# Performance work log

Measured on AMD Instinct MI355X. Metric: run time of the kernel, lower is better.

Reference implementation:

```python
import jax, jax.numpy as jnp
import numpy as np

# Mamba2 defaults (mamba_ssm): d_state=64, d_conv=4, expand=2, headdim=64, ngroups=1
D_MODEL = 512
D_STATE = 64
D_CONV = 4
EXPAND = 2
HEADDIM = 64
D_INNER = EXPAND * D_MODEL            # 1024
NHEADS = D_INNER // HEADDIM           # 16
CONV_DIM = D_INNER + 2 * D_STATE      # 1152
D_IN_PROJ = 2 * D_INNER + 2 * D_STATE + NHEADS  # 2192
BATCH, SEQLEN, CHUNK = 4, 4096, 64


def setup_inputs() -> dict:
    key = jax.random.key(0)
    ks = jax.random.split(key, 8)
    return {
        "x": jax.random.normal(ks[0], (BATCH, SEQLEN, D_MODEL), jnp.float32),
        "ln_w": jnp.ones((D_MODEL,), jnp.float32),
        "ln_b": jnp.zeros((D_MODEL,), jnp.float32),
        "in_w": jax.random.normal(ks[1], (D_MODEL, D_IN_PROJ), jnp.float32) * (D_MODEL ** -0.5),
        "conv_w": jax.random.normal(ks[2], (CONV_DIM, D_CONV), jnp.float32) * (D_CONV ** -0.5),
        "conv_b": jnp.zeros((CONV_DIM,), jnp.float32),
        "dt_bias": jnp.log(jnp.expm1(jax.random.uniform(ks[3], (NHEADS,), jnp.float32, 0.001, 0.1))),
        "A_log": jnp.log(jax.random.uniform(ks[4], (NHEADS,), jnp.float32, 1.0, 16.0)),
        "D": jnp.ones((NHEADS,), jnp.float32),
        "rms_w": jnp.ones((D_INNER,), jnp.float32),
        "out_w": jax.random.normal(ks[5], (D_INNER, D_MODEL), jnp.float32) * (D_INNER ** -0.5),
    }


def _layernorm(x, w, b, eps=1e-5):
    mu = jnp.mean(x, axis=-1, keepdims=True)
    var = jnp.mean((x - mu) ** 2, axis=-1, keepdims=True)
    return (x - mu) * jax.lax.rsqrt(var + eps) * w + b


def _causal_dwconv(x, w, b):  # x [B,L,C], w [C,K], b [C]
    K = w.shape[1]
    xp = jnp.pad(x, ((0, 0), (K - 1, 0), (0, 0)))
    L = x.shape[1]
    out = sum(xp[:, k:k + L, :] * w[None, None, :, k] for k in range(K))
    return out + b


def _ssd(xh, dt, Bm, Cm, A):
    # Chunked SSD (Mamba2 algorithm). xh [B,L,H,P], dt [B,L,H], Bm/Cm [B,L,N], A [H] (negative)
    b, l, h, p = xh.shape
    nc, cs = l // CHUNK, CHUNK
    Xd = (xh * dt[..., None]).reshape(b, nc, cs, h, p)
    Bc = Bm.reshape(b, nc, cs, -1)
    Cc = Cm.reshape(b, nc, cs, -1)
    Ac = (dt * A).reshape(b, nc, cs, h).transpose(0, 3, 1, 2)  # [B,H,nC,cs]
    Acum = jnp.cumsum(Ac, axis=-1)                              # [B,H,nC,cs]
    # intra-chunk (diagonal blocks)
    mask = jnp.tril(jnp.ones((cs, cs), bool))
    seg = Acum[..., :, None] - Acum[..., None, :]               # [B,H,nC,cs,cs]
    Lmat = jnp.where(mask, jnp.exp(jnp.where(mask, seg, 0.0)), 0.0)
    Y_diag = jnp.einsum('bcln,bcsn,bhcls,bcshp->bclhp', Cc, Bc, Lmat, Xd)
    # per-chunk end states
    decay = jnp.exp(Acum[..., -1:] - Acum)                      # [B,H,nC,cs]
    states = jnp.einsum('bcln,bhcl,bclhp->bchpn', Bc, decay, Xd)  # [B,nC,H,P,N]
    chunk_decay = jnp.exp(Acum[..., -1])                        # [B,H,nC]
    def step(s, inp):
        st_c, dec_c = inp
        prev = s
        s = s * dec_c[..., None, None] + st_c
        return s, prev
    _, prev = jax.lax.scan(
        step,
        jnp.zeros((b, h, p, Bc.shape[-1]), xh.dtype),
        (states.transpose(1, 0, 2, 3, 4), chunk_decay.transpose(2, 0, 1)),
    )
    prev = prev.transpose(1, 0, 2, 3, 4)                        # [B,nC,H,P,N]
    Y_off = jnp.einsum('bcln,bchpn,bhcl->bclhp', Cc, prev, jnp.exp(Acum))
    return (Y_diag + Y_off).reshape(b, l, h, p)


def reference(x, ln_w, ln_b, in_w, conv_w, conv_b, dt_bias, A_log, D, rms_w, out_w):
    b, l, _ = x.shape
    h = _layernorm(x, ln_w, ln_b)
    zxbcdt = h @ in_w                                           # [B,L,D_IN_PROJ]
    z = zxbcdt[..., :D_INNER]
    xBC = zxbcdt[..., D_INNER:D_INNER + CONV_DIM]
    dt = jax.nn.softplus(zxbcdt[..., -NHEADS:] + dt_bias)       # [B,L,H]
    xBC = jax.nn.silu(_causal_dwconv(xBC, conv_w, conv_b))
    xs = xBC[..., :D_INNER]
    Bm = xBC[..., D_INNER:D_INNER + D_STATE]
    Cm = xBC[..., D_INNER + D_STATE:]
    xh = xs.reshape(b, l, NHEADS, HEADDIM)
    A = -jnp.exp(A_log)                                         # [H]
    y = _ssd(xh, dt, Bm, Cm, A) + xh * D[None, None, :, None]
    y = y.reshape(b, l, D_INNER)
    # gated RMSNorm: rmsnorm(y * silu(z)) * rms_w
    g = y * jax.nn.silu(z)
    g = g * jax.lax.rsqrt(jnp.mean(g * g, axis=-1, keepdims=True) + 1e-5) * rms_w
    out = g @ out_w
    # dropout in eval mode = identity, drop_path=0 = identity
    return x + out
```

## Files before the change

### kernel.cpp

```cpp
#include <hip/hip_runtime.h>
#include <hip/hip_bf16.h>
#include <cstddef>

#define BATCH  4
#define SEQL   4096
#define DM     512
#define DIP    2192
#define DIPP   2304
#define DI     1024
#define DST    64
#define NH     16
#define HD     64
#define CONVD  1152
#define NROWS  (BATCH*SEQL)

typedef __attribute__((ext_vector_type(8))) short short8;
typedef __attribute__((ext_vector_type(4))) float f32x4;

__device__ __forceinline__ float silu_f(float v){ return v/(1.f+__expf(-v)); }

__device__ __forceinline__ unsigned short bf16_rne(float x){
  unsigned u = __float_as_uint(x);
  unsigned r = u + 0x7FFFu + ((u>>16)&1u);
  return (unsigned short)(r>>16);
}
__device__ __forceinline__ float bf16_to_f(unsigned short h){
  return __uint_as_float(((unsigned)h)<<16);
}

__global__ __launch_bounds__(256)
void k_stats(const float* __restrict__ x, float* __restrict__ stats){
  __shared__ float sm[8];
  int row = blockIdx.x, t = threadIdx.x;
  const float* xr = x + (size_t)row*DM;
  float v0 = xr[t], v1 = xr[t+256];
  float s = v0+v1, s2 = v0*v0+v1*v1;
  for(int o=32;o;o>>=1){ s += __shfl_down(s,o); s2 += __shfl_down(s2,o); }
  if((t&63)==0){ sm[t>>6]=s; sm[4+(t>>6)]=s2; }
  __syncthreads();
  if(t==0){
    float su = sm[0]+sm[1]+sm[2]+sm[3];
    float sq = sm[4]+sm[5]+sm[6]+sm[7];
    float mu = su*(1.f/DM);
    float rs = rsqrtf(sq*(1.f/DM) - mu*mu + 1e-5f);
    stats[row*2] = mu; stats[row*2+1] = rs;
  }
}

__global__ void k_wsplit(const float* __restrict__ src, unsigned short* __restrict__ dh,
                         unsigned short* __restrict__ dl, int K, int N){
  __shared__ float sm[32][33];
  int tx = threadIdx.x, ty = threadIdx.y;
  int n0 = blockIdx.x*32, k0 = blockIdx.y*32;
  #pragma unroll
  for(int j=0;j<4;j++){
    int k = k0+ty+j*8, n = n0+tx;
    sm[ty+j*8][tx] = (k<K && n<N) ? src[(size_t)k*N+n] : 0.f;
  }
  __syncthreads();
  #pragma unroll
  for(int j=0;j<4;j++){
    int n = n0+ty+j*8, k = k0+tx;
    float v = sm[tx][ty+j*8];
    unsigned short hh = bf16_rne(v);
    dh[(size_t)n*K+k] = hh;
    dl[(size_t)n*K+k] = bf16_rne(v - bf16_to_f(hh));
  }
}

__global__ __launch_bounds__(256)
void k_gemm_in(const float* __restrict__ x, const float* __restrict__ stats,
               const float* __restrict__ lnw, const float* __restrict__ lnb,
               const unsigned short* __restrict__ Bhg, const unsigned short* __restrict__ Blg,
               float* __restrict__ z, float* __restrict__ xbc){
  __shared__ unsigned short Ah[128][72], Al[128][72], Bh[128][72], Bl[128][72];
  const int ntn = DIPP/128;
  int bid = blockIdx.x;
  int tm = bid / ntn, tn = bid % ntn;
  int t = threadIdx.x, lane = t&63, wave = t>>6;
  int wr = (wave>>1)*64, wc = (wave&1)*64, fr = lane&15;
  f32x4 zero = {0.f,0.f,0.f,0.f};
  f32x4 acc[4][4];
  #pragma unroll
  for(int m=0;m<4;m++)
    #pragma unroll
    for(int n=0;n<4;n++) acc[m][n]=zero;
  const int arow = tm*128, bcol = tn*128;
  for(int k0=0; k0<DM; k0+=64){
    __syncthreads();
    #pragma unroll
    for(int i=0;i<8;i++){
      int idx = t + i*256;
      int r = idx>>4, cq = (idx&15)*4;
      int grow = arow + r;
      f32x4 xv = *(const f32x4*)(x + (size_t)grow*DM + k0 + cq);
      float mu = stats[grow*2], rsd = stats[grow*2+1];
      f32x4 wv = *(const f32x4*)(lnw + k0 + cq);
      f32x4 bv = *(const f32x4*)(lnb + k0 + cq);
      #pragma unroll
      for(int j=0;j<4;j++){
        float v = (xv[j]-mu)*rsd*wv[j] + bv[j];
        unsigned short hh = bf16_rne(v);
        Ah[r][cq+j] = hh;
        Al[r][cq+j] = bf16_rne(v - bf16_to_f(hh));
      }
    }
    #pragma unroll
    for(int i=0;i<4;i++){
      int idx = t + i*256;
      int r = idx>>3, c8 = (idx&7)*8;
      *(short8*)(&Bh[r][c8]) = *(const short8*)(Bhg + (size_t)(bcol+r)*DM + k0 + c8);
      *(short8*)(&Bl[r][c8]) = *(const short8*)(Blg + (size_t)(bcol+r)*DM + k0 + c8);
    }
    __syncthreads();
    #pragma unroll
    for(int kk=0;kk<2;kk++){
      int fk = kk*32 + ((lane>>4)<<3);
      short8 afh[4], afl[4], bfh[4], bfl[4];
      #pragma unroll
      for(int m=0;m<4;m++){
        afh[m] = *(const short8*)(&Ah[wr+m*16+fr][fk]);
        afl[m] = *(const short8*)(&Al[wr+m*16+fr][fk]);
      }
      #pragma unroll
      for(int n=0;n<4;n++){
        bfh[n] = *(const short8*)(&Bh[wc+n*16+fr][fk]);
        bfl[n] = *(const short8*)(&Bl[wc+n*16+fr][fk]);
      }
      #pragma unroll
      for(int m=0;m<4;m++)
        #pragma unroll
        for(int n=0;n<4;n++){
          acc[m][n] = __builtin_amdgcn_mfma_f32_16x16x32_bf16(afh[m], bfh[n], acc[m][n], 0,0,0);
          acc[m][n] = __builtin_amdgcn_mfma_f32_16x16x32_bf16(afh[m], bfl[n], acc[m][n], 0,0,0);
          acc[m][n] = __builtin_amdgcn_mfma_f32_16x16x32_bf16(afl[m], bfh[n], acc[m][n], 0,0,0);
        }
    }
  }
  int fq = (lane>>4)*4;
  #pragma unroll
  for(int m=0;m<4;m++)
    #pragma unroll
    for(int n=0;n<4;n++)
      #pragma unroll
      for(int j=0;j<4;j++){
        int row = arow + wr + m*16 + fq + j;
        int col = bcol + wc + n*16 + fr;
        float v = acc[m][n][j];
        if(col < DI) z[(size_t)row*DI + col] = v;
        else if(col < DI+CONVD) xbc[(size_t)row*CONVD + (col-DI)] = v;
      }
}

__global__ __launch_bounds__(256)
void k_gemm_out(const float* __restrict__ G, const unsigned short* __restrict__ Bhg,
                const unsigned short* __restrict__ Blg, const float* __restrict__ resid,
                float* __restrict__ outp){
  __shared__ unsigned short Ah[128][72], Al[128][72], Bh[128][72], Bl[128][72];
  const int ntn = DM/128;
  int bid = blockIdx.x;
  int tm = bid / ntn, tn = bid % ntn;
  int t = threadIdx.x, lane = t&63, wave = t>>6;
  int wr = (wave>>1)*64, wc = (wave&1)*64, fr = lane&15;
  f32x4 zero = {0.f,0.f,0.f,0.f};
  f32x4 acc[4][4];
  #pragma unroll
  for(int m=0;m<4;m++)
    #pragma unroll
    for(int n=0;n<4;n++) acc[m][n]=zero;
  const int arow = tm*128, bcol = tn*128;
  for(int k0=0; k0<DI; k0+=64){
    __syncthreads();
    int h = k0>>6;
    #pragma unroll
    for(int i=0;i<8;i++){
      int idx = t + i*256;
      int r = idx>>4, cq = (idx&15)*4;
      int grow = arow + r;
      int bb = grow>>12, cc = (grow>>6)&63, lin = grow&63;
      size_t base = ((size_t)((bb*64+cc)*NH + h))*4096 + (size_t)lin*64;
      f32x4 gv = *(const f32x4*)(G + base + cq);
      #pragma unroll
      for(int j=0;j<4;j++){
        unsigned short hh = bf16_rne(gv[j]);
        Ah[r][cq+j] = hh;
        Al[r][cq+j] = bf16_rne(gv[j] - bf16_to_f(hh));
      }
    }
    #pragma unroll
    for(int i=0;i<4;i++){
      int idx = t + i*256;
      int r = idx>>3, c8 = (idx&7)*8;
      *(short8*)(&Bh[r][c8]) = *(const short8*)(Bhg + (size_t)(bcol+r)*DI + k0 + c8);
      *(short8*)(&Bl[r][c8]) = *(const short8*)(Blg + (size_t)(bcol+r)*DI + k0 + c8);
    }
    __syncthreads();
    #pragma unroll
    for(int kk=0;kk<2;kk++){
      int fk = kk*32 + ((lane>>4)<<3);
      short8 afh[4], afl[4], bfh[4], bfl[4];
      #pragma unroll
      for(int m=0;m<4;m++){
        afh[m] = *(const short8*)(&Ah[wr+m*16+fr][fk]);
        afl[m] = *(const short8*)(&Al[wr+m*16+fr][fk]);
      }
      #pragma unroll
      for(int n=0;n<4;n++){
        bfh[n] = *(const short8*)(&Bh[wc+n*16+fr][fk]);
        bfl[n] = *(const short8*)(&Bl[wc+n*16+fr][fk]);
      }
      #pragma unroll
      for(int m=0;m<4;m++)
        #pragma unroll
        for(int n=0;n<4;n++){
          acc[m][n] = __builtin_amdgcn_mfma_f32_16x16x32_bf16(afh[m], bfh[n], acc[m][n], 0,0,0);
          acc[m][n] = __builtin_amdgcn_mfma_f32_16x16x32_bf16(afh[m], bfl[n], acc[m][n], 0,0,0);
          acc[m][n] = __builtin_amdgcn_mfma_f32_16x16x32_bf16(afl[m], bfh[n], acc[m][n], 0,0,0);
        }
    }
  }
  int fq = (lane>>4)*4;
  #pragma unroll
  for(int m=0;m<4;m++)
    #pragma unroll
    for(int n=0;n<4;n++)
      #pragma unroll
      for(int j=0;j<4;j++){
        int row = arow + wr + m*16 + fq + j;
        int col = bcol + wc + n*16 + fr;
        outp[(size_t)row*DM + col] = acc[m][n][j] + resid[(size_t)row*DM + col];
      }
}

__global__ __launch_bounds__(256)
void k_dt(const float* __restrict__ x, const float* __restrict__ stats,
          const float* __restrict__ lnw, const float* __restrict__ lnb,
          const float* __restrict__ in_w, const float* __restrict__ dt_bias,
          float* __restrict__ dtp){
  __shared__ float red[64];
  int row = blockIdx.x, t = threadIdx.x;
  float mu = stats[row*2], rs = stats[row*2+1];
  float a[16];
  #pragma unroll
  for(int j=0;j<16;j++) a[j]=0.f;
  #pragma unroll
  for(int i=0;i<2;i++){
    int k = t + i*256;
    float hv = (x[(size_t)row*DM + k]-mu)*rs*lnw[k] + lnb[k];
    const float* wr2 = in_w + (size_t)k*DIP + (DIP-NH);
    #pragma unroll
    for(int j=0;j<16;j++) a[j] += hv * wr2[j];
  }
  for(int o=32;o;o>>=1){
    #pragma unroll
    for(int j=0;j<16;j++) a[j] += __shfl_down(a[j],o);
  }
  if((t&63)==0){
    #pragma unroll
    for(int j=0;j<16;j++) red[(t>>6)*16+j] = a[j];
  }
  __syncthreads();
  if(t<16){
    float v = red[t] + red[16+t] + red[32+t] + red[48+t] + dt_bias[t];
    dtp[(size_t)row*NH + t] = (v > 20.f) ? v : log1pf(__expf(v));
  }
}

__global__ __launch_bounds__(256)
void k_convBC(const float* __restrict__ xbc, const float* __restrict__ cw,
              const float* __restrict__ cb, float* __restrict__ bcc){
  int gid = blockIdx.x*256 + threadIdx.x;
  int c4 = gid & 31, row = gid >> 5;
  int c = c4*4;
  int lb = row & (SEQL-1);
  const float* base = xbc + (size_t)row*CONVD + DI + c;
  f32x4 w0 = *(const f32x4*)(cw + (size_t)(DI+c+0)*4);
  f32x4 w1 = *(const f32x4*)(cw + (size_t)(DI+c+1)*4);
  f32x4 w2 = *(const f32x4*)(cw + (size_t)(DI+c+2)*4);
  f32x4 w3 = *(const f32x4*)(cw + (size_t)(DI+c+3)*4);
  f32x4 r = { cb[DI+c], cb[DI+c+1], cb[DI+c+2], cb[DI+c+3] };
  #pragma unroll
  for(int k=0;k<4;k++){
    if(lb-3+k >= 0){
      f32x4 xv = *(const f32x4*)(base + (long)(k-3)*CONVD);
      r.x += xv.x*w0[k]; r.y += xv.y*w1[k]; r.z += xv.z*w2[k]; r.w += xv.w*w3[k];
    }
  }
  r.x = silu_f(r.x); r.y = silu_f(r.y); r.z = silu_f(r.z); r.w = silu_f(r.w);
  *(f32x4*)(bcc + (size_t)row*128 + c) = r;
}

__global__ void k_acum(const float* __restrict__ dtp, const float* __restrict__ A_log,
                       float* __restrict__ acum, float* __restrict__ cdec){
  int bh = blockIdx.x;
  int h = bh & 15;
  int c = blockIdx.y, l = threadIdx.x;
  int row = (bh>>4)*SEQL + c*64 + l;
  float a = -__expf(A_log[h]);
  float v = dtp[(size_t)row*NH + h] * a;
  for(int o=1;o<64;o<<=1){ float u = __shfl_up(v,o); if(l>=o) v += u; }
  acum[(size_t)bh*SEQL + c*64 + l] = v;
  if(l==63) cdec[bh*64 + c] = __expf(v);
}

__global__ __launch_bounds__(256)
void k_states(const float* __restrict__ xbc, const float* __restrict__ bcc,
              const float* __restrict__ dtp, const float* __restrict__ acum,
              const float* __restrict__ cw, const float* __restrict__ cb,
              float* __restrict__ S){
  int h = blockIdx.x, bc = blockIdx.y;
  int b = bc >> 6, c = bc & 63;
  __shared__ float Bd[64][68];
  __shared__ float Xs[64][68];
  __shared__ float raw[67*64];
  __shared__ f32x4 wc4[64];
  __shared__ float cbv[64], acs[64], dts[64];
  int t = threadIdx.x;
  if(t < 64){
    acs[t] = acum[((size_t)(b*NH+h))*SEQL + c*64 + t];
    dts[t] = dtp[(size_t)(b*SEQL + c*64 + t)*NH + h];
    wc4[t] = *(const f32x4*)(cw + (size_t)(h*HD + t)*4);
    cbv[t] = cb[h*HD + t];
  }
  __syncthreads();
  #pragma unroll
  for(int i=0;i<4;i++){
    int idx = t + i*256;
    int l = idx>>4, n4 = (idx&15)*4;
    f32x4 bv = *(const f32x4*)(bcc + (size_t)(b*SEQL + c*64 + l)*128 + n4);
    float dec = __expf(acs[63] - acs[l]);
    *(f32x4*)&Bd[l][n4] = bv * dec;
  }
  #pragma unroll
  for(int i=0;i<5;i++){
    int idx = t + i*256;
    if(idx < 67*16){
      int rr = idx>>4, p4 = (idx&15)*4;
      int wb = c*64 - 3 + rr;
      f32x4 xv = {0.f,0.f,0.f,0.f};
      if(wb >= 0) xv = *(const f32x4*)(xbc + (size_t)(b*SEQL + wb)*CONVD + h*HD + p4);
      *(f32x4*)&raw[rr*64 + p4] = xv;
    }
  }
  __syncthreads();
  {
    int l = t>>2, q = t&3;
    float dtv = dts[l];
    #pragma unroll
    for(int jj=0;jj<16;jj++){
      int p = q*16 + jj;
      f32x4 w = wc4[p];
      float a = cbv[p] + raw[(l+0)*64+p]*w.x + raw[(l+1)*64+p]*w.y
              + raw[(l+2)*64+p]*w.z + raw[(l+3)*64+p]*w.w;
      Xs[l][p] = silu_f(a) * dtv;
    }
  }
  __syncthreads();
  int n = t>>2, p0 = (t&3)*16;
  f32x4 a0={0.f,0.f,0.f,0.f}, a1=a0, a2=a0, a3=a0;
  #pragma unroll 2
  for(int ll=0; ll<64; ll++){
    float bnd = Bd[ll][n];
    const float* xp = &Xs[ll][p0];
    a0 += bnd * *(const f32x4*)(xp);
    a1 += bnd * *(const f32x4*)(xp+4);
    a2 += bnd * *(const f32x4*)(xp+8);
    a3 += bnd * *(const f32x4*)(xp+12);
  }
  float* op = S + ((size_t)(bc*NH + h))*4096 + n*64 + p0;
  *(f32x4*)(op)    = a0;
  *(f32x4*)(op+4)  = a1;
  *(f32x4*)(op+8)  = a2;
  *(f32x4*)(op+12) = a3;
}

__global__ void k_scan(float* __restrict__ S, const float* __restrict__ cdec){
  int g = blockIdx.x*256 + threadIdx.x;
  int bh = g >> 12;
  int pn = g & 4095;
  int b = bh >> 4, h = bh & 15;
  const float* cd = cdec + bh*64;
  float s = 0.f;
  for(int c=0;c<64;c++){
    size_t idx = ((size_t)((b*64 + c)*NH + h))*4096 + pn;
    float v = S[idx];
    float d = cd[c];
    S[idx] = s;
    s = s*d + v;
  }
}

__global__ __launch_bounds__(256)
void k_y(const float* __restrict__ xbc, const float* __restrict__ bcc,
         const float* __restrict__ dtp, const float* __restrict__ acum,
         const float* __restrict__ cw, const float* __restrict__ cb,
         const float* __restrict__ Dp, float* __restrict__ Sreg){
  int h = blockIdx.x, bc = blockIdx.y;
  int b = bc >> 6, c = bc & 63;
  __shared__ float Cs[64][68];
  __shared__ float BM[64][68];
  __shared__ float Xr[64][68];
  __shared__ float PsRaw[64*68];
  __shared__ f32x4 wc4[64];
  __shared__ float cbv[64], acs[64], dts[64];
  int t = threadIdx.x;
  float* Sslot = Sreg + ((size_t)(bc*NH + h))*4096;
  if(t < 64){
    acs[t] = acum[((size_t)(b*NH+h))*SEQL + c*64 + t];
    dts[t] = dtp[(size_t)(b*SEQL + c*64 + t)*NH + h];
    wc4[t] = *(const f32x4*)(cw + (size_t)(h*HD + t)*4);
    cbv[t] = cb[h*HD + t];
  }
  #pragma unroll
  for(int i=0;i<4;i++){
    int idx = t + i*256;
    int l = idx>>4, n4 = (idx&15)*4;
    const float* bp = bcc + (size_t)(b*SEQL + c*64 + l)*128;
    *(f32x4*)&BM[l][n4] = *(const f32x4*)(bp + n4);
    *(f32x4*)&Cs[l][n4] = *(const f32x4*)(bp + 64 + n4);
  }
  #pragma unroll
  for(int i=0;i<5;i++){
    int idx = t + i*256;
    if(idx < 67*16){
      int rr = idx>>4, p4 = (idx&15)*4;
      int wb = c*64 - 3 + rr;
      f32x4 xv = {0.f,0.f,0.f,0.f};
      if(wb >= 0) xv = *(const f32x4*)(xbc + (size_t)(b*SEQL + wb)*CONVD + h*HD + p4);
      *(f32x4*)&PsRaw[rr*64 + p4] = xv;
    }
  }
  __syncthreads();
  {
    int l = t>>2, q = t&3;
    #pragma unroll
    for(int jj=0;jj<16;jj++){
      int p = q*16 + jj;
      f32x4 w = wc4[p];
      float a = cbv[p] + PsRaw[(l+0)*64+p]*w.x + PsRaw[(l+1)*64+p]*w.y
              + PsRaw[(l+2)*64+p]*w.z + PsRaw[(l+3)*64+p]*w.w;
      Xr[l][p] = silu_f(a);
    }
  }
  __syncthreads();
  int gl = t & 63, s0 = (t>>6)*16;
  float g[16];
  #pragma unroll
  for(int j=0;j<16;j++) g[j]=0.f;
  #pragma unroll 1
  for(int n4=0;n4<64;n4+=4){
    f32x4 cv = *(const f32x4*)&Cs[gl][n4];
    #pragma unroll
    for(int j=0;j<16;j++){
      f32x4 bv = *(const f32x4*)&BM[s0+j][n4];
      g[j] += cv.x*bv.x + cv.y*bv.y + cv.z*bv.z + cv.w*bv.w;
    }
  }
  __syncthreads();
  {
    float aclg = acs[gl];
    #pragma unroll
    for(int j=0;j<16;j++){
      int s = s0 + j;
      BM[gl][s] = (s <= gl) ? g[j]*__expf(aclg - acs[s])*dts[s] : 0.f;
    }
  }
  #pragma unroll
  for(int i=0;i<4;i++){
    int idx = t + i*256;
    int s = idx>>4, p4 = (idx&15)*4;
    f32x4 pv = *(const f32x4*)(Sslot + s*64 + p4);
    *(f32x4*)&PsRaw[s*68 + p4] = pv;
  }
  __syncthreads();
  {
    int l = t>>2, p0 = (t&3)*16;
    float eal = __expf(acs[l]);
    float Dh = Dp[h];
    const float* xl = &Xr[l][p0];
    f32x4 a0 = Dh * *(const f32x4*)(xl);
    f32x4 a1 = Dh * *(const f32x4*)(xl+4);
    f32x4 a2 = Dh * *(const f32x4*)(xl+8);
    f32x4 a3 = Dh * *(const f32x4*)(xl+12);
    #pragma unroll 2
    for(int s=0;s<64;s++){
      float m = BM[l][s];
      const float* xp = &Xr[s][p0];
      a0 += m * *(const f32x4*)(xp);
      a1 += m * *(const f32x4*)(xp+4);
      a2 += m * *(const f32x4*)(xp+8);
      a3 += m * *(const f32x4*)(xp+12);
    }
    #pragma unroll 2
    for(int s=0;s<64;s++){
      float cv = eal * Cs[l][s];
      const float* pp = &PsRaw[s*68 + p0];
      a0 += cv * *(const f32x4*)(pp);
      a1 += cv * *(const f32x4*)(pp+4);
      a2 += cv * *(const f32x4*)(pp+8);
      a3 += cv * *(const f32x4*)(pp+12);
    }
    float* yp = Sslot + l*64 + p0;
    *(f32x4*)(yp)    = a0;
    *(f32x4*)(yp+4)  = a1;
    *(f32x4*)(yp+8)  = a2;
    *(f32x4*)(yp+12) = a3;
  }
}

__global__ __launch_bounds__(256)
void k_gate(float* __restrict__ Sreg, const float* __restrict__ z,
            const float* __restrict__ rms_w){
  __shared__ float sm[4];
  int row = blockIdx.x, t = threadIdx.x;
  int b = row>>12, cc = (row>>6)&63, lin = row&63;
  int h = t>>4, p = (t&15)*4;
  float* gp = Sreg + ((size_t)((b*64+cc)*NH + h))*4096 + (size_t)lin*64 + p;
  f32x4 yv = *(const f32x4*)gp;
  f32x4 zv = *(const f32x4*)(z + (size_t)row*DI + t*4);
  f32x4 gv;
  gv.x = yv.x * silu_f(zv.x);
  gv.y = yv.y * silu_f(zv.y);
  gv.z = yv.z * silu_f(zv.z);
  gv.w = yv.w * silu_f(zv.w);
  float ss = gv.x*gv.x + gv.y*gv.y + gv.z*gv.z + gv.w*gv.w;
  for(int o=32;o;o>>=1) ss += __shfl_down(ss,o);
  if((t&63)==0) sm[t>>6] = ss;
  __syncthreads();
  float tot = sm[0]+sm[1]+sm[2]+sm[3];
  float scale = rsqrtf(tot*(1.f/DI) + 1e-5f);
  f32x4 wv = *(const f32x4*)(rms_w + t*4);
  gv.x *= scale*wv.x; gv.y *= scale*wv.y; gv.z *= scale*wv.z; gv.w *= scale*wv.w;
  *(f32x4*)gp = gv;
}

extern "C" void kernel_launch(void* const* d_in, const int* in_sizes, int n_in,
                              void* d_out, int out_size, void* d_ws, size_t ws_size,
                              hipStream_t stream) {
  const float* x      = (const float*)d_in[0];
  const float* ln_w   = (const float*)d_in[1];
  const float* ln_b   = (const float*)d_in[2];
  const float* in_w   = (const float*)d_in[3];
  const float* conv_w = (const float*)d_in[4];
  const float* conv_b = (const float*)d_in[5];
  const float* dt_b   = (const float*)d_in[6];
  const float* A_log  = (const float*)d_in[7];
  const float* Dp     = (const float*)d_in[8];
  const float* rms_w  = (const float*)d_in[9];
  const float* out_w  = (const float*)d_in[10];
  float* out = (float*)d_out;
  char* ws = (char*)d_ws;

  size_t o = 0;
  float* stats = (float*)(ws+o);           o += (size_t)NROWS*2*4;
  unsigned short* w1h = (unsigned short*)(ws+o); o += (size_t)DIPP*DM*2;
  unsigned short* w1l = (unsigned short*)(ws+o); o += (size_t)DIPP*DM*2;
  unsigned short* w2h = (unsigned short*)(ws+o); o += (size_t)DM*DI*2;
  unsigned short* w2l = (unsigned short*)(ws+o); o += (size_t)DM*DI*2;
  float* z    = (float*)(ws+o);            o += (size_t)NROWS*DI*4;
  float* xbc  = (float*)(ws+o);            o += (size_t)NROWS*CONVD*4;
  float* dtp  = (float*)(ws+o);            o += (size_t)NROWS*NH*4;
  float* acum = (float*)(ws+o);            o += (size_t)BATCH*NH*SEQL*4;
  float* cdec = (float*)(ws+o);            o += (size_t)BATCH*NH*64*4;
  float* bcc  = (float*)(ws+o);            o += (size_t)NROWS*128*4;
  float* Sreg = (float*)(ws+o);            o += (size_t)BATCH*64*NH*4096*4;
  if(o > ws_size) return;

  k_stats<<<NROWS, 256, 0, stream>>>(x, stats);
  k_wsplit<<<dim3(DIPP/32, DM/32), dim3(32,8), 0, stream>>>(in_w,  w1h, w1l, DM, DIP);
  k_wsplit<<<dim3(DM/32,  DI/32), dim3(32,8), 0, stream>>>(out_w, w2h, w2l, DI, DM);
  k_gemm_in<<<(NROWS/128)*(DIPP/128), 256, 0, stream>>>(x, stats, ln_w, ln_b, w1h, w1l, z, xbc);
  k_dt<<<NROWS, 256, 0, stream>>>(x, stats, ln_w, ln_b, in_w, dt_b, dtp);
  k_convBC<<<(NROWS*32)/256, 256, 0, stream>>>(xbc, conv_w, conv_b, bcc);
  k_acum<<<dim3(BATCH*NH, 64), 64, 0, stream>>>(dtp, A_log, acum, cdec);
  k_states<<<dim3(NH, BATCH*64), 256, 0, stream>>>(xbc, bcc, dtp, acum, conv_w, conv_b, Sreg);
  k_scan<<<(BATCH*NH*4096)/256, 256, 0, stream>>>(Sreg, cdec);
  k_y<<<dim3(NH, BATCH*64), 256, 0, stream>>>(xbc, bcc, dtp, acum, conv_w, conv_b, Dp, Sreg);
  k_gate<<<NROWS, 256, 0, stream>>>(Sreg, z, rms_w);
  k_gemm_out<<<(NROWS/128)*(DM/128), 256, 0, stream>>>(Sreg, w2h, w2l, x, out);
}
```

Baseline: 782.3 us.

## Precompute bf16 hi/lo operand planes and trim padded GEMM columns

LayerNorm output is now normalised and split into bf16 hi/lo planes once in the stats kernel, and the gate kernel writes bf16 hi/lo planes in row-major order. Both GEMMs therefore load ready-made short8 tiles instead of converting fp32 per tile. The in-projection N dimension drops from 2304 to 2176, cutting padded tiles. The change also adds workgroup-id swizzling and LDS row padding of 76. Workspace buffers are aliased (Ai reuses Sreg, gh/gl reuse xbc), which relies on the launch ordering leaving those buffers dead at the right time.

```diff
diff --git a/kernel.cpp b/kernel.cpp
--- a/kernel.cpp
+++ b/kernel.cpp
@@ -6,7 +6,7 @@
 #define SEQL   4096
 #define DM     512
 #define DIP    2192
-#define DIPP   2304
+#define NIP    2176
 #define DI     1024
 #define DST    64
 #define NH     16
@@ -16,6 +16,7 @@
 
 typedef __attribute__((ext_vector_type(8))) short short8;
 typedef __attribute__((ext_vector_type(4))) float f32x4;
+typedef __attribute__((ext_vector_type(4))) unsigned short u16x4;
 
 __device__ __forceinline__ float silu_f(float v){ return v/(1.f+__expf(-v)); }
 
@@ -29,7 +30,9 @@
 }
 
 __global__ __launch_bounds__(256)
-void k_stats(const float* __restrict__ x, float* __restrict__ stats){
+void k_stats(const float* __restrict__ x, const float* __restrict__ lnw,
+             const float* __restrict__ lnb, float* __restrict__ stats,
+             unsigned short* __restrict__ Ai){
   __shared__ float sm[8];
   int row = blockIdx.x, t = threadIdx.x;
   const float* xr = x + (size_t)row*DM;
@@ -38,44 +41,52 @@
   for(int o=32;o;o>>=1){ s += __shfl_down(s,o); s2 += __shfl_down(s2,o); }
   if((t&63)==0){ sm[t>>6]=s; sm[4+(t>>6)]=s2; }
   __syncthreads();
-  if(t==0){
-    float su = sm[0]+sm[1]+sm[2]+sm[3];
-    float sq = sm[4]+sm[5]+sm[6]+sm[7];
-    float mu = su*(1.f/DM);
-    float rs = rsqrtf(sq*(1.f/DM) - mu*mu + 1e-5f);
-    stats[row*2] = mu; stats[row*2+1] = rs;
-  }
+  float su = sm[0]+sm[1]+sm[2]+sm[3];
+  float sq = sm[4]+sm[5]+sm[6]+sm[7];
+  float mu = su*(1.f/DM);
+  float rs = rsqrtf(sq*(1.f/DM) - mu*mu + 1e-5f);
+  if(t==0){ stats[row*2]=mu; stats[row*2+1]=rs; }
+  unsigned short* ap = Ai + (size_t)row*2*DM;
+  float a0 = (v0-mu)*rs*lnw[t] + lnb[t];
+  unsigned short h0 = bf16_rne(a0);
+  ap[t] = h0; ap[DM+t] = bf16_rne(a0 - bf16_to_f(h0));
+  float a1 = (v1-mu)*rs*lnw[t+256] + lnb[t+256];
+  unsigned short h1 = bf16_rne(a1);
+  ap[t+256] = h1; ap[DM+t+256] = bf16_rne(a1 - bf16_to_f(h1));
 }
 
 __global__ void k_wsplit(const float* __restrict__ src, unsigned short* __restrict__ dh,
-                         unsigned short* __restrict__ dl, int K, int N){
+                         unsigned short* __restrict__ dl, int K, int N, int srcStride){
   __shared__ float sm[32][33];
   int tx = threadIdx.x, ty = threadIdx.y;
   int n0 = blockIdx.x*32, k0 = blockIdx.y*32;
   #pragma unroll
   for(int j=0;j<4;j++){
     int k = k0+ty+j*8, n = n0+tx;
-    sm[ty+j*8][tx] = (k<K && n<N) ? src[(size_t)k*N+n] : 0.f;
+    sm[ty+j*8][tx] = (k<K && n<N) ? src[(size_t)k*srcStride+n] : 0.f;
   }
   __syncthreads();
   #pragma unroll
   for(int j=0;j<4;j++){
     int n = n0+ty+j*8, k = k0+tx;
-    float v = sm[tx][ty+j*8];
-    unsigned short hh = bf16_rne(v);
-    dh[(size_t)n*K+k] = hh;
-    dl[(size_t)n*K+k] = bf16_rne(v - bf16_to_f(hh));
-  }
-}
-
-__global__ __launch_bounds__(256)
-void k_gemm_in(const float* __restrict__ x, const float* __restrict__ stats,
-               const float* __restrict__ lnw, const float* __restrict__ lnb,
+    if(n < N){
+      float v = sm[tx][ty+j*8];
+      unsigned short hh = bf16_rne(v);
+      dh[(size_t)n*K+k] = hh;
+      dl[(size_t)n*K+k] = bf16_rne(v - bf16_to_f(hh));
+    }
+  }
+}
+
+__global__ __launch_bounds__(256)
+void k_gemm_in(const unsigned short* __restrict__ Ai,
                const unsigned short* __restrict__ Bhg, const unsigned short* __restrict__ Blg,
                float* __restrict__ z, float* __restrict__ xbc){
-  __shared__ unsigned short Ah[128][72], Al[128][72], Bh[128][72], Bl[128][72];
-  const int ntn = DIPP/128;
-  int bid = blockIdx.x;
+  __shared__ unsigned short Ah[128][76], Al[128][76], Bh[128][76], Bl[128][76];
+  const int ntn = NIP/128;
+  int nwg = gridDim.x;
+  int bid0 = blockIdx.x;
+  int bid = (bid0 & 7)*(nwg>>3) + (bid0>>3);
   int tm = bid / ntn, tn = bid % ntn;
   int t = threadIdx.x, lane = t&63, wave = t>>6;
   int wr = (wave>>1)*64, wc = (wave&1)*64, fr = lane&15;
@@ -86,24 +97,15 @@
     #pragma unroll
     for(int n=0;n<4;n++) acc[m][n]=zero;
   const int arow = tm*128, bcol = tn*128;
+  int plane = (t>>3)&1;
+  unsigned short* Adst = plane ? &Al[0][0] : &Ah[0][0];
   for(int k0=0; k0<DM; k0+=64){
     __syncthreads();
     #pragma unroll
     for(int i=0;i<8;i++){
-      int idx = t + i*256;
-      int r = idx>>4, cq = (idx&15)*4;
-      int grow = arow + r;
-      f32x4 xv = *(const f32x4*)(x + (size_t)grow*DM + k0 + cq);
-      float mu = stats[grow*2], rsd = stats[grow*2+1];
-      f32x4 wv = *(const f32x4*)(lnw + k0 + cq);
-      f32x4 bv = *(const f32x4*)(lnb + k0 + cq);
-      #pragma unroll
-      for(int j=0;j<4;j++){
-        float v = (xv[j]-mu)*rsd*wv[j] + bv[j];
-        unsigned short hh = bf16_rne(v);
-        Ah[r][cq+j] = hh;
-        Al[r][cq+j] = bf16_rne(v - bf16_to_f(hh));
-      }
+      int r = (t>>4) + i*16, c8 = (t&7)*8;
+      *(short8*)(Adst + r*76 + c8) =
+        *(const short8*)(Ai + ((size_t)(arow+r)*2 + plane)*DM + k0 + c8);
     }
     #pragma unroll
     for(int i=0;i<4;i++){
@@ -148,17 +150,19 @@
         int col = bcol + wc + n*16 + fr;
         float v = acc[m][n][j];
         if(col < DI) z[(size_t)row*DI + col] = v;
-        else if(col < DI+CONVD) xbc[(size_t)row*CONVD + (col-DI)] = v;
+        else xbc[(size_t)row*CONVD + (col-DI)] = v;
       }
 }
 
 __global__ __launch_bounds__(256)
-void k_gemm_out(const float* __restrict__ G, const unsigned short* __restrict__ Bhg,
-                const unsigned short* __restrict__ Blg, const float* __restrict__ resid,
-                float* __restrict__ outp){
-  __shared__ unsigned short Ah[128][72], Al[128][72], Bh[128][72], Bl[128][72];
+void k_gemm_out(const unsigned short* __restrict__ gh, const unsigned short* __restrict__ gl,
+                const unsigned short* __restrict__ Bhg, const unsigned short* __restrict__ Blg,
+                const float* __restrict__ resid, float* __restrict__ outp){
+  __shared__ unsigned short Ah[128][76], Al[128][76], Bh[128][76], Bl[128][76];
   const int ntn = DM/128;
-  int bid = blockIdx.x;
+  int nwg = gridDim.x;
+  int bid0 = blockIdx.x;
+  int bid = (bid0 & 7)*(nwg>>3) + (bid0>>3);
   int tm = bid / ntn, tn = bid % ntn;
   int t = threadIdx.x, lane = t&63, wave = t>>6;
   int wr = (wave>>1)*64, wc = (wave&1)*64, fr = lane&15;
@@ -169,23 +173,16 @@
     #pragma unroll
     for(int n=0;n<4;n++) acc[m][n]=zero;
   const int arow = tm*128, bcol = tn*128;
+  int plane = (t>>3)&1;
+  unsigned short* Adst = plane ? &Al[0][0] : &Ah[0][0];
+  const unsigned short* gsrc = plane ? gl : gh;
   for(int k0=0; k0<DI; k0+=64){
     __syncthreads();
-    int h = k0>>6;
     #pragma unroll
     for(int i=0;i<8;i++){
-      int idx = t + i*256;
-      int r = idx>>4, cq = (idx&15)*4;
-      int grow = arow + r;
-      int bb = grow>>12, cc = (grow>>6)&63, lin = grow&63;
-      size_t base = ((size_t)((bb*64+cc)*NH + h))*4096 + (size_t)lin*64;
-      f32x4 gv = *(const f32x4*)(G + base + cq);
-      #pragma unroll
-      for(int j=0;j<4;j++){
-        unsigned short hh = bf16_rne(gv[j]);
-        Ah[r][cq+j] = hh;
-        Al[r][cq+j] = bf16_rne(gv[j] - bf16_to_f(hh));
-      }
+      int r = (t>>4) + i*16, c8 = (t&7)*8;
+      *(short8*)(Adst + r*76 + c8) =
+        *(const short8*)(gsrc + (size_t)(arow+r)*DI + k0 + c8);
     }
     #pragma unroll
     for(int i=0;i<4;i++){
@@ -509,13 +506,14 @@
 }
 
 __global__ __launch_bounds__(256)
-void k_gate(float* __restrict__ Sreg, const float* __restrict__ z,
-            const float* __restrict__ rms_w){
+void k_gate(const float* __restrict__ Sreg, const float* __restrict__ z,
+            const float* __restrict__ rms_w, unsigned short* __restrict__ gh,
+            unsigned short* __restrict__ gl){
   __shared__ float sm[4];
   int row = blockIdx.x, t = threadIdx.x;
   int b = row>>12, cc = (row>>6)&63, lin = row&63;
   int h = t>>4, p = (t&15)*4;
-  float* gp = Sreg + ((size_t)((b*64+cc)*NH + h))*4096 + (size_t)lin*64 + p;
+  const float* gp = Sreg + ((size_t)((b*64+cc)*NH + h))*4096 + (size_t)lin*64 + p;
   f32x4 yv = *(const f32x4*)gp;
   f32x4 zv = *(const f32x4*)(z + (size_t)row*DI + t*4);
   f32x4 gv;
@@ -530,8 +528,16 @@
   float tot = sm[0]+sm[1]+sm[2]+sm[3];
   float scale = rsqrtf(tot*(1.f/DI) + 1e-5f);
   f32x4 wv = *(const f32x4*)(rms_w + t*4);
-  gv.x *= scale*wv.x; gv.y *= scale*wv.y; gv.z *= scale*wv.z; gv.w *= scale*wv.w;
-  *(f32x4*)gp = gv;
+  float o0 = gv.x*scale*wv.x, o1 = gv.y*scale*wv.y;
+  float o2 = gv.z*scale*wv.z, o3 = gv.w*scale*wv.w;
+  u16x4 hv, lv;
+  unsigned short hh;
+  hh = bf16_rne(o0); hv[0]=hh; lv[0]=bf16_rne(o0-bf16_to_f(hh));
+  hh = bf16_rne(o1); hv[1]=hh; lv[1]=bf16_rne(o1-bf16_to_f(hh));
+  hh = bf16_rne(o2); hv[2]=hh; lv[2]=bf16_rne(o2-bf16_to_f(hh));
+  hh = bf16_rne(o3); hv[3]=hh; lv[3]=bf16_rne(o3-bf16_to_f(hh));
+  *(u16x4*)(gh + (size_t)row*DI + t*4) = hv;
+  *(u16x4*)(gl + (size_t)row*DI + t*4) = lv;
 }
 
 extern "C" void kernel_launch(void* const* d_in, const int* in_sizes, int n_in,
@@ -553,8 +559,8 @@
 
   size_t o = 0;
   float* stats = (float*)(ws+o);           o += (size_t)NROWS*2*4;
-  unsigned short* w1h = (unsigned short*)(ws+o); o += (size_t)DIPP*DM*2;
-  unsigned short* w1l = (unsigned short*)(ws+o); o += (size_t)DIPP*DM*2;
+  unsigned short* w1h = (unsigned short*)(ws+o); o += (size_t)NIP*DM*2;
+  unsigned short* w1l = (unsigned short*)(ws+o); o += (size_t)NIP*DM*2;
   unsigned short* w2h = (unsigned short*)(ws+o); o += (size_t)DM*DI*2;
   unsigned short* w2l = (unsigned short*)(ws+o); o += (size_t)DM*DI*2;
   float* z    = (float*)(ws+o);            o += (size_t)NROWS*DI*4;
@@ -566,16 +572,20 @@
   float* Sreg = (float*)(ws+o);            o += (size_t)BATCH*64*NH*4096*4;
   if(o > ws_size) return;
 
-  k_stats<<<NROWS, 256, 0, stream>>>(x, stats);
-  k_wsplit<<<dim3(DIPP/32, DM/32), dim3(32,8), 0, stream>>>(in_w,  w1h, w1l, DM, DIP);
-  k_wsplit<<<dim3(DM/32,  DI/32), dim3(32,8), 0, stream>>>(out_w, w2h, w2l, DI, DM);
-  k_gemm_in<<<(NROWS/128)*(DIPP/128), 256, 0, stream>>>(x, stats, ln_w, ln_b, w1h, w1l, z, xbc);
+  unsigned short* Ai = (unsigned short*)Sreg;
+  unsigned short* gh = (unsigned short*)xbc;
+  unsigned short* gl = gh + (size_t)NROWS*DI;
+
+  k_stats<<<NROWS, 256, 0, stream>>>(x, ln_w, ln_b, stats, Ai);
+  k_wsplit<<<dim3(NIP/32, DM/32), dim3(32,8), 0, stream>>>(in_w,  w1h, w1l, DM, NIP, DIP);
+  k_wsplit<<<dim3(DM/32,  DI/32), dim3(32,8), 0, stream>>>(out_w, w2h, w2l, DI, DM, DM);
+  k_gemm_in<<<(NROWS/128)*(NIP/128), 256, 0, stream>>>(Ai, w1h, w1l, z, xbc);
   k_dt<<<NROWS, 256, 0, stream>>>(x, stats, ln_w, ln_b, in_w, dt_b, dtp);
   k_convBC<<<(NROWS*32)/256, 256, 0, stream>>>(xbc, conv_w, conv_b, bcc);
   k_acum<<<dim3(BATCH*NH, 64), 64, 0, stream>>>(dtp, A_log, acum, cdec);
   k_states<<<dim3(NH, BATCH*64), 256, 0, stream>>>(xbc, bcc, dtp, acum, conv_w, conv_b, Sreg);
   k_scan<<<(BATCH*NH*4096)/256, 256, 0, stream>>>(Sreg, cdec);
   k_y<<<dim3(NH, BATCH*64), 256, 0, stream>>>(xbc, bcc, dtp, acum, conv_w, conv_b, Dp, Sreg);
-  k_gate<<<NROWS, 256, 0, stream>>>(Sreg, z, rms_w);
-  k_gemm_out<<<(NROWS/128)*(DM/128), 256, 0, stream>>>(Sreg, w2h, w2l, x, out);
-}
+  k_gate<<<NROWS, 256, 0, stream>>>(Sreg, z, rms_w, gh, gl);
+  k_gemm_out<<<(NROWS/128)*(DM/128), 256, 0, stream>>>(gh, gl, w2h, w2l, x, out);
+}
```

Measured after the change: 677.9 us. 1.15x faster.
